# Kernel tuning notes

Hardware: AMD Instinct MI355X
Metric: run time of the kernel (lower is better)

The kernel has to match this reference:

```python
import jax, jax.numpy as jnp
import numpy as np

T, B, U = 64, 2048, 1024


def setup_inputs() -> dict:
    key = jax.random.key(0)
    ks = jax.random.split(key, 7)
    inputs = jax.random.normal(ks[0], (T, B, 1), dtype=jnp.float32)
    x1_0 = jax.random.normal(ks[1], (B, 1), dtype=jnp.float32)
    x2_0 = jax.random.normal(ks[2], (B, 1), dtype=jnp.float32)
    c0 = jax.random.normal(ks[3], (B, U), dtype=jnp.float32)
    kernel = jax.random.normal(ks[4], (1, 2 * U), dtype=jnp.float32) * 0.05
    # orthogonal-ish recurrent kernel, scaled for stability
    recurrent_kernel = jax.random.normal(ks[5], (U, 2 * U), dtype=jnp.float32) * (1.0 / np.sqrt(U))
    # unit_forget_bias: ones for the f gate, zeros for the c gate
    bias = jnp.concatenate([jnp.ones((U,), jnp.float32), jnp.zeros((U,), jnp.float32)])
    output_kernel = jax.random.normal(ks[6], (U, 1), dtype=jnp.float32) * 0.05
    return {"inputs": inputs, "x1_0": x1_0, "x2_0": x2_0, "c0": c0,
            "kernel": kernel, "recurrent_kernel": recurrent_kernel,
            "bias": bias, "output_kernel": output_kernel}


def reference(inputs, x1_0, x2_0, c0, kernel, recurrent_kernel, bias, output_kernel):
    U = c0.shape[-1]
    Kf, Kc = kernel[:, :U], kernel[:, U:2 * U]          # [1,U] each
    Rf, Rc = recurrent_kernel[:, :U], recurrent_kernel[:, U:2 * U]  # [U,U]
    bf, bc = bias[:U], bias[U:2 * U]

    def step(carry, inp):
        x1, x2, h = carry                 # x1,x2: [B,1]; h (= c_{t-1}): [B,U]
        x_f = h @ Rf + x1 @ Kf + bf       # [B,U]
        x_c = h @ Rc + x1 @ Kc + bc       # [B,U]
        f = jax.nn.sigmoid(x_f)
        c = f * h + (1.0 - f) * jnp.tanh(x_c)
        x1_new = x1 + x2                  # double-integrator position update
        x2_new = x2 + inp * (c @ output_kernel)  # velocity driven by scalar input * readout
        return (x1_new, x2_new, c), x1_new

    _, outputs = jax.lax.scan(step, (x1_0, x2_0, c0), inputs)
    return outputs  # [T, B, 1]
```

## Files before the change

### kernel.cpp

```cpp
#include <hip/hip_runtime.h>
#include <hip/hip_bf16.h>

#define T_STEPS 64
#define B_DIM 2048
#define U_DIM 1024
#define KITERS 32

typedef __attribute__((ext_vector_type(8))) _Float16 h8;
typedef __attribute__((ext_vector_type(4))) float f4;

#define WAIT_VM0 __builtin_amdgcn_s_waitcnt(0x0F70)

__device__ __forceinline__ void async_cp16(const _Float16* g, _Float16* l) {
    __builtin_amdgcn_global_load_lds((const __attribute__((address_space(1))) void*)g,
                                     (__attribute__((address_space(3))) void*)l,
                                     16, 0, 0);
}


__global__ void transpose_R(const float* __restrict__ R, _Float16* __restrict__ Rt) {
    __shared__ float tile[32][33];
    int nb = blockIdx.x * 32;
    int kb = blockIdx.y * 32;
    int tx = threadIdx.x, ty = threadIdx.y;
    #pragma unroll
    for (int i = ty; i < 32; i += 8)
        tile[i][tx] = R[(size_t)(kb + i) * (2 * U_DIM) + nb + tx];
    __syncthreads();
    #pragma unroll
    for (int i = ty; i < 32; i += 8)
        Rt[(size_t)(nb + i) * U_DIM + kb + tx] = (_Float16)tile[tx][i];
}

__global__ void init_state(const float* __restrict__ c0, _Float16* __restrict__ h0,
                           float* __restrict__ y, unsigned* __restrict__ bar) {
    int i = blockIdx.x * 256 + threadIdx.x;
    h0[i] = (_Float16)c0[i];
    if (i < 3 * B_DIM) y[i] = 0.f;
    if (i < 256) bar[i] = 0u;
}

#define ALOAD1(dst, addr, OFFSTR) \
    asm volatile("global_load_dwordx4 %0, %1, off offset:" OFFSTR " sc0" \
                 : "=&v"(dst) : "v"(addr) : "memory")

#define ALOADG(S, OFFSTR) do { \
    ALOAD1(afq[S][0], am[0], OFFSTR); \
    ALOAD1(afq[S][1], am[1], OFFSTR); } while (0)

#define MFMA8(S) do { \
    __builtin_amdgcn_s_setprio(1); \
    _Pragma("unroll") \
    for (int mt = 0; mt < 2; ++mt) { \
        accF[mt][0] = __builtin_amdgcn_mfma_f32_16x16x32_f16(afq[S][mt], bff0, accF[mt][0], 0, 0, 0); \
        accF[mt][1] = __builtin_amdgcn_mfma_f32_16x16x32_f16(afq[S][mt], bff1, accF[mt][1], 0, 0, 0); \
        accC[mt][0] = __builtin_amdgcn_mfma_f32_16x16x32_f16(afq[S][mt], bfc0, accC[mt][0], 0, 0, 0); \
        accC[mt][1] = __builtin_amdgcn_mfma_f32_16x16x32_f16(afq[S][mt], bfc1, accC[mt][1], 0, 0, 0); \
    } \
    __builtin_amdgcn_s_setprio(0); } while (0)

#define KSTEP(KT, S, PFOFF) do { \
    h8 bff0 = *(const h8*)&lB[0][0][KT][rdoff]; \
    h8 bff1 = *(const h8*)&lB[0][1][KT][rdoff]; \
    h8 bfc0 = *(const h8*)&lB[1][0][KT][rdoff]; \
    h8 bfc1 = *(const h8*)&lB[1][1][KT][rdoff]; \
    __builtin_amdgcn_s_waitcnt(0x0F76); \
    __builtin_amdgcn_sched_barrier(0); \
    MFMA8(S); \
    ALOADG(S, PFOFF); } while (0)

#define KTAIL(KT, S, WENC) do { \
    h8 bff0 = *(const h8*)&lB[0][0][KT][rdoff]; \
    h8 bff1 = *(const h8*)&lB[0][1][KT][rdoff]; \
    h8 bfc0 = *(const h8*)&lB[1][0][KT][rdoff]; \
    h8 bfc1 = *(const h8*)&lB[1][1][KT][rdoff]; \
    __builtin_amdgcn_s_waitcnt(WENC); \
    __builtin_amdgcn_sched_barrier(0); \
    MFMA8(S); } while (0)

__global__ __launch_bounds__(512, 2) void persist(
    _Float16* __restrict__ h0, _Float16* __restrict__ h1,
    const _Float16* __restrict__ Rt,
    const float* __restrict__ x1_0, const float* __restrict__ x2_0,
    const float* __restrict__ kern, const float* __restrict__ bias,
    const float* __restrict__ okern,
    float* y,
    const float* __restrict__ inputs,
    float* __restrict__ out,
    unsigned* bar)
{
    __shared__ __align__(16) _Float16 lB[2][2][KITERS][512];
    __shared__ __align__(16) _Float16 lC[256 * 40];
    __shared__ float x1s[256];

    const int tid    = threadIdx.x;
    const int wid    = tid >> 6;
    const int lane   = tid & 63;
    const int lane15 = lane & 15;
    const int quad   = lane >> 4;
    const int bid    = blockIdx.x;
    const int b0     = (bid & 7) * 256;
    const int u0     = (bid >> 3) * 32;
    const bool ub0   = (bid >> 3) == 0;
    const int wrow   = wid * 32;
    const int srow   = lane >> 2;
    const int schnk  = (((lane & 3) ^ (srow & 3) ^ ((srow >> 2) & 3)) * 8);
    const int sw     = ((quad ^ (lane15 & 3) ^ ((lane15 >> 2) & 3)) * 8);
    const int rdoff  = lane15 * 32 + sw;
    const int myb    = b0 + tid;
    unsigned* ctr   = &bar[(bid & 7) * 32];
    unsigned* xmask = &bar[(bid & 7) * 32 + 8];

    #pragma unroll
    for (int gate = 0; gate < 2; ++gate)
        #pragma unroll
        for (int nt = 0; nt < 2; ++nt)
            #pragma unroll
            for (int i = 0; i < 4; ++i) {
                const int kt = wid + i * 8;
                async_cp16(Rt + (size_t)(gate * U_DIM + u0 + nt * 16 + srow) * U_DIM + kt * 32 + schnk,
                           &lB[gate][nt][kt][0]);
            }

    int* flag = (int*)x1s;
    if (tid == 0) {
        const unsigned xcc = (unsigned)__builtin_amdgcn_s_getreg(63508) & 31u;
        __hip_atomic_fetch_or(xmask, 1u << xcc, __ATOMIC_RELAXED, __HIP_MEMORY_SCOPE_AGENT);
        __hip_atomic_fetch_add(ctr, 1u, __ATOMIC_RELAXED, __HIP_MEMORY_SCOPE_AGENT);
        while (__hip_atomic_load(ctr, __ATOMIC_RELAXED, __HIP_MEMORY_SCOPE_AGENT) < 32u)
            __builtin_amdgcn_s_sleep(1);
        const unsigned m = __hip_atomic_load(xmask, __ATOMIC_RELAXED, __HIP_MEMORY_SCOPE_AGENT);
        *flag = (__popc(m) == 1) ? 1 : 0;
    }
    __syncthreads();
    const bool xcd_pure = (*flag != 0);

    float kf[2], kc[2], bf_[2], bc_[2], ok_[2];
    #pragma unroll
    for (int nt = 0; nt < 2; ++nt) {
        const int u = u0 + nt * 16 + lane15;
        kf[nt]  = kern[u];        kc[nt]  = kern[U_DIM + u];
        bf_[nt] = bias[u];        bc_[nt] = bias[U_DIM + u];
        ok_[nt] = okern[u];
    }

    _Float16 hv[2][2][4];
    #pragma unroll
    for (int mt = 0; mt < 2; ++mt)
        #pragma unroll
        for (int nt = 0; nt < 2; ++nt)
            #pragma unroll
            for (int reg = 0; reg < 4; ++reg)
                hv[mt][nt][reg] = h0[(size_t)(b0 + wrow + mt * 16 + quad * 4 + reg) * U_DIM
                                     + u0 + nt * 16 + lane15];

    float x1r = 0.f, x2r = 0.f;
    if (tid < 256) { x1r = x1_0[myb]; x2r = x2_0[myb]; }

    WAIT_VM0;
    __syncthreads();

    _Float16* hA_ = h0;
    _Float16* hB_ = h1;

    #pragma unroll 1
    for (int t = 0; t < T_STEPS; ++t) {
        if (tid < 256) {
            if (t > 0) {
                const float ip = inputs[(size_t)(t - 1) * B_DIM + myb];
                const float yp = __hip_atomic_load(&y[((t + 2) % 3) * B_DIM + myb],
                                                   __ATOMIC_RELAXED, __HIP_MEMORY_SCOPE_AGENT);
                x1r = x1r + x2r;
                x2r = x2r + ip * yp;
            }
            if (ub0) {
                if (t > 0) out[(size_t)(t - 1) * B_DIM + myb] = x1r;
                if (t == T_STEPS - 1)
                    out[(size_t)(T_STEPS - 1) * B_DIM + myb] = x1r + x2r;
                else
                    __hip_atomic_store(&y[((t + 1) % 3) * B_DIM + myb], 0.f,
                                       __ATOMIC_RELAXED, __HIP_MEMORY_SCOPE_AGENT);
            }
            x1s[tid] = x1r;
        }
        if (t == T_STEPS - 1) break;

        __syncthreads();

        unsigned long long am[2];
        {
            const _Float16* ab = hA_ + (size_t)(b0 + wrow + lane15) * U_DIM + quad * 8;
            am[0] = (unsigned long long)ab;
            am[1] = (unsigned long long)(ab + (size_t)16 * U_DIM);
        }

        f4 accF[2][2], accC[2][2];
        #pragma unroll
        for (int mt = 0; mt < 2; ++mt)
            #pragma unroll
            for (int nt = 0; nt < 2; ++nt) {
                accF[mt][nt] = (f4){0.f, 0.f, 0.f, 0.f};
                accC[mt][nt] = (f4){0.f, 0.f, 0.f, 0.f};
            }

        h8 afq[4][2];
        ALOADG(0, "0"); ALOADG(1, "64"); ALOADG(2, "128"); ALOADG(3, "192");
        KSTEP(0, 0, "256");   KSTEP(1, 1, "320");   KSTEP(2, 2, "384");   KSTEP(3, 3, "448");
        KSTEP(4, 0, "512");   KSTEP(5, 1, "576");   KSTEP(6, 2, "640");   KSTEP(7, 3, "704");
        KSTEP(8, 0, "768");   KSTEP(9, 1, "832");   KSTEP(10, 2, "896");  KSTEP(11, 3, "960");
        KSTEP(12, 0, "1024"); KSTEP(13, 1, "1088"); KSTEP(14, 2, "1152"); KSTEP(15, 3, "1216");
        KSTEP(16, 0, "1280"); KSTEP(17, 1, "1344"); KSTEP(18, 2, "1408"); KSTEP(19, 3, "1472");
        KSTEP(20, 0, "1536"); KSTEP(21, 1, "1600"); KSTEP(22, 2, "1664"); KSTEP(23, 3, "1728");
        KSTEP(24, 0, "1792"); KSTEP(25, 1, "1856"); KSTEP(26, 2, "1920"); KSTEP(27, 3, "1984");
        KTAIL(28, 0, 0x0F76); KTAIL(29, 1, 0x0F74); KTAIL(30, 2, 0x0F72); KTAIL(31, 3, 0x0F70);

        float* ycur = y + (t % 3) * B_DIM;
        #pragma unroll
        for (int mt = 0; mt < 2; ++mt) {
            const int rlb = wrow + mt * 16 + quad * 4;
            float psum[4] = {0.f, 0.f, 0.f, 0.f};
            #pragma unroll
            for (int nt = 0; nt < 2; ++nt) {
                const int ul = nt * 16 + lane15;
                #pragma unroll
                for (int reg = 0; reg < 4; ++reg) {
                    const int rl = rlb + reg;
                    const float x1 = x1s[rl];
                    const float xf = accF[mt][nt][reg] + x1 * kf[nt] + bf_[nt];
                    const float xc = accC[mt][nt][reg] + x1 * kc[nt] + bc_[nt];
                    const float fg = 1.f / (1.f + __expf(-xf));
                    const float th = 1.f - 2.f / (1.f + __expf(2.f * xc));
                    const float cv = fg * (float)hv[mt][nt][reg] + (1.f - fg) * th;
                    hv[mt][nt][reg] = (_Float16)cv;
                    lC[rl * 40 + ul] = (_Float16)cv;
                    psum[reg] += cv * ok_[nt];
                }
            }
            #pragma unroll
            for (int reg = 0; reg < 4; ++reg) {
                float s = psum[reg];
                s += __shfl_xor(s, 1);
                s += __shfl_xor(s, 2);
                s += __shfl_xor(s, 4);
                s += __shfl_xor(s, 8);
                if (lane15 == 0) atomicAdd(&ycur[b0 + rlb + reg], s);
            }
        }

        __syncthreads();
        #pragma unroll
        for (int j = 0; j < 2; ++j) {
            const int idx = j * 512 + tid;
            const int row = idx >> 2;
            const int col = idx & 3;
            *(uint4*)&hB_[(size_t)(b0 + row) * U_DIM + u0 + col * 8] =
                *(const uint4*)&lC[row * 40 + col * 8];
        }

        { _Float16* tmp = hA_; hA_ = hB_; hB_ = tmp; }

        if (!xcd_pure) __builtin_amdgcn_fence(__ATOMIC_RELEASE, "agent");
        __syncthreads();
        if (tid == 0) {
            __hip_atomic_fetch_add(ctr, 1u, __ATOMIC_RELAXED, __HIP_MEMORY_SCOPE_AGENT);
            while (__hip_atomic_load(ctr, __ATOMIC_RELAXED, __HIP_MEMORY_SCOPE_AGENT)
                   < 32u * (unsigned)(t + 2))
                __builtin_amdgcn_s_sleep(1);
        }
        __syncthreads();
        if (!xcd_pure) __builtin_amdgcn_fence(__ATOMIC_ACQUIRE, "agent");
    }
}

extern "C" void kernel_launch(void* const* d_in, const int* in_sizes, int n_in,
                              void* d_out, int out_size, void* d_ws, size_t ws_size,
                              hipStream_t stream) {
    const float* inputs = (const float*)d_in[0];
    const float* x1_0   = (const float*)d_in[1];
    const float* x2_0   = (const float*)d_in[2];
    const float* c0     = (const float*)d_in[3];
    const float* kern   = (const float*)d_in[4];
    const float* rker   = (const float*)d_in[5];
    const float* bias   = (const float*)d_in[6];
    const float* okern  = (const float*)d_in[7];
    float* out = (float*)d_out;

    _Float16* Rt = (_Float16*)d_ws;
    _Float16* h0 = Rt + (size_t)2 * U_DIM * U_DIM;
    _Float16* h1 = h0 + (size_t)B_DIM * U_DIM;
    float* y = (float*)(h1 + (size_t)B_DIM * U_DIM);
    unsigned* bar = (unsigned*)(y + 3 * B_DIM);

    transpose_R<<<dim3(64, 32), dim3(32, 8), 0, stream>>>(rker, Rt);
    init_state<<<dim3(B_DIM * U_DIM / 256), dim3(256), 0, stream>>>(c0, h0, y, bar);
    persist<<<dim3(256), dim3(512), 0, stream>>>(h0, h1, Rt, x1_0, x2_0,
                                                 kern, bias, okern, y, inputs, out, bar);
}
```

Baseline: 1.412 ms.

## Retile warps to 64x16 per wave, drop sc0 loads, add L1 invalidate

Each wave now covers a 64-row by 16-unit tile instead of 32x32. That halves the LDS B-fragment reads per k-step and drops the XOR swizzle, but doubles the global A (h) loads per wave, and the prefetch wait counts are adjusted to match. The A loads lose the sc0 cache bit so they can hit in L1. To keep that correct when all blocks share one XCD, a buffer_inv is added after the grid barrier. The risks are more redundant global A traffic per block and LDS bank conflicts from the now unswizzled B layout.

New measurement: 2.591 ms. +83.5%, slower.

```diff
diff --git a/kernel.cpp b/kernel.cpp
--- a/kernel.cpp
+++ b/kernel.cpp
@@ -41,39 +41,35 @@
 }
 
 #define ALOAD1(dst, addr, OFFSTR) \
-    asm volatile("global_load_dwordx4 %0, %1, off offset:" OFFSTR " sc0" \
+    asm volatile("global_load_dwordx4 %0, %1, off offset:" OFFSTR \
                  : "=&v"(dst) : "v"(addr) : "memory")
 
 #define ALOADG(S, OFFSTR) do { \
     ALOAD1(afq[S][0], am[0], OFFSTR); \
-    ALOAD1(afq[S][1], am[1], OFFSTR); } while (0)
+    ALOAD1(afq[S][1], am[1], OFFSTR); \
+    ALOAD1(afq[S][2], am[2], OFFSTR); \
+    ALOAD1(afq[S][3], am[3], OFFSTR); } while (0)
 
 #define MFMA8(S) do { \
     __builtin_amdgcn_s_setprio(1); \
     _Pragma("unroll") \
-    for (int mt = 0; mt < 2; ++mt) { \
-        accF[mt][0] = __builtin_amdgcn_mfma_f32_16x16x32_f16(afq[S][mt], bff0, accF[mt][0], 0, 0, 0); \
-        accF[mt][1] = __builtin_amdgcn_mfma_f32_16x16x32_f16(afq[S][mt], bff1, accF[mt][1], 0, 0, 0); \
-        accC[mt][0] = __builtin_amdgcn_mfma_f32_16x16x32_f16(afq[S][mt], bfc0, accC[mt][0], 0, 0, 0); \
-        accC[mt][1] = __builtin_amdgcn_mfma_f32_16x16x32_f16(afq[S][mt], bfc1, accC[mt][1], 0, 0, 0); \
+    for (int mt = 0; mt < 4; ++mt) { \
+        accF[mt] = __builtin_amdgcn_mfma_f32_16x16x32_f16(afq[S][mt], bff, accF[mt], 0, 0, 0); \
+        accC[mt] = __builtin_amdgcn_mfma_f32_16x16x32_f16(afq[S][mt], bfc, accC[mt], 0, 0, 0); \
     } \
     __builtin_amdgcn_s_setprio(0); } while (0)
 
 #define KSTEP(KT, S, PFOFF) do { \
-    h8 bff0 = *(const h8*)&lB[0][0][KT][rdoff]; \
-    h8 bff1 = *(const h8*)&lB[0][1][KT][rdoff]; \
-    h8 bfc0 = *(const h8*)&lB[1][0][KT][rdoff]; \
-    h8 bfc1 = *(const h8*)&lB[1][1][KT][rdoff]; \
-    __builtin_amdgcn_s_waitcnt(0x0F76); \
+    h8 bff = *(const h8*)&lB[0][ns][KT][lane8]; \
+    h8 bfc = *(const h8*)&lB[1][ns][KT][lane8]; \
+    __builtin_amdgcn_s_waitcnt(0x0F7C); \
     __builtin_amdgcn_sched_barrier(0); \
     MFMA8(S); \
     ALOADG(S, PFOFF); } while (0)
 
 #define KTAIL(KT, S, WENC) do { \
-    h8 bff0 = *(const h8*)&lB[0][0][KT][rdoff]; \
-    h8 bff1 = *(const h8*)&lB[0][1][KT][rdoff]; \
-    h8 bfc0 = *(const h8*)&lB[1][0][KT][rdoff]; \
-    h8 bfc1 = *(const h8*)&lB[1][1][KT][rdoff]; \
+    h8 bff = *(const h8*)&lB[0][ns][KT][lane8]; \
+    h8 bfc = *(const h8*)&lB[1][ns][KT][lane8]; \
     __builtin_amdgcn_s_waitcnt(WENC); \
     __builtin_amdgcn_sched_barrier(0); \
     MFMA8(S); } while (0)
@@ -98,28 +94,28 @@
     const int lane   = tid & 63;
     const int lane15 = lane & 15;
     const int quad   = lane >> 4;
+    const int lane8  = lane * 8;
     const int bid    = blockIdx.x;
     const int b0     = (bid & 7) * 256;
     const int u0     = (bid >> 3) * 32;
     const bool ub0   = (bid >> 3) == 0;
-    const int wrow   = wid * 32;
-    const int srow   = lane >> 2;
-    const int schnk  = (((lane & 3) ^ (srow & 3) ^ ((srow >> 2) & 3)) * 8);
-    const int sw     = ((quad ^ (lane15 & 3) ^ ((lane15 >> 2) & 3)) * 8);
-    const int rdoff  = lane15 * 32 + sw;
+    const int ms     = wid >> 1;
+    const int ns     = wid & 1;
+    const int wrow   = ms * 64;
     const int myb    = b0 + tid;
     unsigned* ctr   = &bar[(bid & 7) * 32];
     unsigned* xmask = &bar[(bid & 7) * 32 + 8];
 
     #pragma unroll
-    for (int gate = 0; gate < 2; ++gate)
-        #pragma unroll
-        for (int nt = 0; nt < 2; ++nt)
+    for (int g = 0; g < 2; ++g)
+        #pragma unroll
+        for (int nsr = 0; nsr < 2; ++nsr)
             #pragma unroll
             for (int i = 0; i < 4; ++i) {
                 const int kt = wid + i * 8;
-                async_cp16(Rt + (size_t)(gate * U_DIM + u0 + nt * 16 + srow) * U_DIM + kt * 32 + schnk,
-                           &lB[gate][nt][kt][0]);
+                async_cp16(Rt + (size_t)(g * U_DIM + u0 + nsr * 16 + lane15) * U_DIM
+                              + kt * 32 + quad * 8,
+                           &lB[g][nsr][kt][0]);
             }
 
     int* flag = (int*)x1s;
@@ -135,24 +131,19 @@
     __syncthreads();
     const bool xcd_pure = (*flag != 0);
 
-    float kf[2], kc[2], bf_[2], bc_[2], ok_[2];
-    #pragma unroll
-    for (int nt = 0; nt < 2; ++nt) {
-        const int u = u0 + nt * 16 + lane15;
-        kf[nt]  = kern[u];        kc[nt]  = kern[U_DIM + u];
-        bf_[nt] = bias[u];        bc_[nt] = bias[U_DIM + u];
-        ok_[nt] = okern[u];
-    }
-
-    _Float16 hv[2][2][4];
-    #pragma unroll
-    for (int mt = 0; mt < 2; ++mt)
-        #pragma unroll
-        for (int nt = 0; nt < 2; ++nt)
-            #pragma unroll
-            for (int reg = 0; reg < 4; ++reg)
-                hv[mt][nt][reg] = h0[(size_t)(b0 + wrow + mt * 16 + quad * 4 + reg) * U_DIM
-                                     + u0 + nt * 16 + lane15];
+    const int ucol = u0 + ns * 16 + lane15;
+    const float kf  = kern[ucol];
+    const float kc  = kern[U_DIM + ucol];
+    const float bf_ = bias[ucol];
+    const float bc_ = bias[U_DIM + ucol];
+    const float ok_ = okern[ucol];
+
+    _Float16 hv[4][4];
+    #pragma unroll
+    for (int mt = 0; mt < 4; ++mt)
+        #pragma unroll
+        for (int reg = 0; reg < 4; ++reg)
+            hv[mt][reg] = h0[(size_t)(b0 + wrow + mt * 16 + quad * 4 + reg) * U_DIM + ucol];
 
     float x1r = 0.f, x2r = 0.f;
     if (tid < 256) { x1r = x1_0[myb]; x2r = x2_0[myb]; }
@@ -187,23 +178,22 @@
 
         __syncthreads();
 
-        unsigned long long am[2];
+        unsigned long long am[4];
         {
             const _Float16* ab = hA_ + (size_t)(b0 + wrow + lane15) * U_DIM + quad * 8;
-            am[0] = (unsigned long long)ab;
-            am[1] = (unsigned long long)(ab + (size_t)16 * U_DIM);
-        }
-
-        f4 accF[2][2], accC[2][2];
-        #pragma unroll
-        for (int mt = 0; mt < 2; ++mt)
-            #pragma unroll
-            for (int nt = 0; nt < 2; ++nt) {
-                accF[mt][nt] = (f4){0.f, 0.f, 0.f, 0.f};
-                accC[mt][nt] = (f4){0.f, 0.f, 0.f, 0.f};
-            }
-
-        h8 afq[4][2];
+            #pragma unroll
+            for (int mt = 0; mt < 4; ++mt)
+                am[mt] = (unsigned long long)(ab + (size_t)mt * 16 * U_DIM);
+        }
+
+        f4 accF[4], accC[4];
+        #pragma unroll
+        for (int mt = 0; mt < 4; ++mt) {
+            accF[mt] = (f4){0.f, 0.f, 0.f, 0.f};
+            accC[mt] = (f4){0.f, 0.f, 0.f, 0.f};
+        }
+
+        h8 afq[4][4];
         ALOADG(0, "0"); ALOADG(1, "64"); ALOADG(2, "128"); ALOADG(3, "192");
         KSTEP(0, 0, "256");   KSTEP(1, 1, "320");   KSTEP(2, 2, "384");   KSTEP(3, 3, "448");
         KSTEP(4, 0, "512");   KSTEP(5, 1, "576");   KSTEP(6, 2, "640");   KSTEP(7, 3, "704");
@@ -212,29 +202,26 @@
         KSTEP(16, 0, "1280"); KSTEP(17, 1, "1344"); KSTEP(18, 2, "1408"); KSTEP(19, 3, "1472");
         KSTEP(20, 0, "1536"); KSTEP(21, 1, "1600"); KSTEP(22, 2, "1664"); KSTEP(23, 3, "1728");
         KSTEP(24, 0, "1792"); KSTEP(25, 1, "1856"); KSTEP(26, 2, "1920"); KSTEP(27, 3, "1984");
-        KTAIL(28, 0, 0x0F76); KTAIL(29, 1, 0x0F74); KTAIL(30, 2, 0x0F72); KTAIL(31, 3, 0x0F70);
+        KTAIL(28, 0, 0x0F7C); KTAIL(29, 1, 0x0F78); KTAIL(30, 2, 0x0F74); KTAIL(31, 3, 0x0F70);
 
         float* ycur = y + (t % 3) * B_DIM;
-        #pragma unroll
-        for (int mt = 0; mt < 2; ++mt) {
+        const int ul = ns * 16 + lane15;
+        #pragma unroll
+        for (int mt = 0; mt < 4; ++mt) {
             const int rlb = wrow + mt * 16 + quad * 4;
-            float psum[4] = {0.f, 0.f, 0.f, 0.f};
-            #pragma unroll
-            for (int nt = 0; nt < 2; ++nt) {
-                const int ul = nt * 16 + lane15;
-                #pragma unroll
-                for (int reg = 0; reg < 4; ++reg) {
-                    const int rl = rlb + reg;
-                    const float x1 = x1s[rl];
-                    const float xf = accF[mt][nt][reg] + x1 * kf[nt] + bf_[nt];
-                    const float xc = accC[mt][nt][reg] + x1 * kc[nt] + bc_[nt];
-                    const float fg = 1.f / (1.f + __expf(-xf));
-                    const float th = 1.f - 2.f / (1.f + __expf(2.f * xc));
-                    const float cv = fg * (float)hv[mt][nt][reg] + (1.f - fg) * th;
-                    hv[mt][nt][reg] = (_Float16)cv;
-                    lC[rl * 40 + ul] = (_Float16)cv;
-                    psum[reg] += cv * ok_[nt];
-                }
+            float psum[4];
+            #pragma unroll
+            for (int reg = 0; reg < 4; ++reg) {
+                const int rl = rlb + reg;
+                const float x1 = x1s[rl];
+                const float xf = accF[mt][reg] + x1 * kf + bf_;
+                const float xc = accC[mt][reg] + x1 * kc + bc_;
+                const float fg = 1.f / (1.f + __expf(-xf));
+                const float th = 1.f - 2.f / (1.f + __expf(2.f * xc));
+                const float cv = fg * (float)hv[mt][reg] + (1.f - fg) * th;
+                hv[mt][reg] = (_Float16)cv;
+                lC[rl * 40 + ul] = (_Float16)cv;
+                psum[reg] = cv * ok_;
             }
             #pragma unroll
             for (int reg = 0; reg < 4; ++reg) {
@@ -268,7 +255,11 @@
                 __builtin_amdgcn_s_sleep(1);
         }
         __syncthreads();
-        if (!xcd_pure) __builtin_amdgcn_fence(__ATOMIC_ACQUIRE, "agent");
+        if (xcd_pure) {
+            asm volatile("buffer_inv" ::: "memory");
+        } else {
+            __builtin_amdgcn_fence(__ATOMIC_ACQUIRE, "agent");
+        }
     }
 }
 
```
